# Optimization experiments

Hardware: AMD Instinct MI355X
Metric: run time of the kernel (lower is better)

Reference implementation:

```python
import jax, jax.numpy as jnp
import numpy as np

N, D, S, K = 4096, 256, 32, 4   # nodes, in_dim(=out_dim), subspace_dim, num_heads
ETA = 0.5
LAMBDA_SPARSE = 0.05
EDGE_P = 0.02  # graph density for the random adjacency mask


def setup_inputs() -> dict:
    key = jax.random.key(0)
    k1, k2, k3 = jax.random.split(key, 3)
    H = jax.random.normal(k1, (N, D), dtype=jnp.float32)
    # binary adjacency mask with self-loops, stored as float (matches torch usage)
    mask = (jax.random.uniform(k2, (N, N)) < EDGE_P).astype(jnp.float32)
    adj_mask = jnp.maximum(mask, jnp.eye(N, dtype=jnp.float32))
    # per-head orthonormal subspace bases U[k] = qr(randn(D,S)) -> [K, D, S]
    raw = jax.random.normal(k3, (K, D, S), dtype=jnp.float32)
    U, _ = jnp.linalg.qr(raw)
    log_precision = jnp.zeros((K, S), dtype=jnp.float32)
    threshold = jnp.full((D,), LAMBDA_SPARSE, dtype=jnp.float32)
    return {"H": H, "adj_mask": adj_mask, "U": U,
            "log_precision": log_precision, "threshold": threshold}


def reference(H, adj_mask, U, log_precision, threshold):
    s = U.shape[-1]
    inv_sqrt_s = 1.0 / jnp.sqrt(jnp.asarray(s, dtype=H.dtype))
    neg = (1.0 - adj_mask) * (-1e9)  # [N, N] additive mask

    # scan over heads keeps peak memory at one [N,N] score matrix at a time
    def head_step(agg, xs):
        Uk, lpk = xs                       # [D,S], [S]
        Z = H @ Uk                         # [N,S]  (= Zk^T in the torch code)
        Zs = Z * jnp.exp(lpk)              # precision-scaled
        scores = (Zs @ Z.T) * inv_sqrt_s + neg   # [N,N]
        alpha = jax.nn.softmax(scores, axis=-1)
        agg = agg + (alpha @ Z) @ Uk.T     # [N,D] == (Uk @ (Zk @ alpha^T))^T
        return agg, None

    agg, _ = jax.lax.scan(head_step, jnp.zeros_like(H), (U, log_precision))
    H_half = H + ETA * agg                 # in_dim == out_dim -> no proj

    # soft threshold
    H_out = jnp.sign(H_half) * jax.nn.relu(jnp.abs(H_half) - threshold[None, :])

    # orthogonality loss: sum_k ||Uk^T Uk - I||_F^2 + sum_{k<l} ||Uk^T Ul||_F^2
    C = jnp.einsum('kda,ldb->klab', U, U)  # [K,K,S,S] gram blocks (K,S small)
    Kh = U.shape[0]
    I = jnp.eye(s, dtype=U.dtype)
    diag_blocks = C[jnp.arange(Kh), jnp.arange(Kh)]          # [K,S,S]
    orth_loss = ((diag_blocks - I) ** 2).sum()
    upper = jnp.triu(jnp.ones((Kh, Kh), dtype=U.dtype), 1)[:, :, None, None]
    orth_loss = orth_loss + ((C ** 2) * upper).sum()
    return H_out, orth_loss
```

## Files before the change

### kernel.cpp

```cpp
#include <hip/hip_runtime.h>
#include <math.h>

constexpr int NN = 4096;
constexpr int DD = 256;
constexpr int SS = 32;
constexpr int KK = 4;
constexpr int MAXN = 192;
constexpr int SEGMAX = 96;
constexpr float ETA = 0.5f;

#define MEMFENCE() __asm__ volatile("" ::: "memory")

__global__ __launch_bounds__(256) void prep_kernel(
    const float* __restrict__ H, const float* __restrict__ U,
    const float* __restrict__ lp, float* __restrict__ Z,
    float* __restrict__ elp, float* __restrict__ lossp) {
  __shared__ float Hl[16][DD];
  __shared__ float red[4];
  const int tid = threadIdx.x;

  if (blockIdx.x < 1024) {
    const int k = blockIdx.x & 3;
    const int n0 = (blockIdx.x >> 2) * 16;

    const float4* H4 = (const float4*)(H + (size_t)n0 * DD);
    float4* Hl4 = (float4*)&Hl[0][0];
    for (int i = tid; i < 16 * DD / 4; i += 256) Hl4[i] = H4[i];
    __syncthreads();

    const int s = tid & 31;
    const int n_l = (tid >> 5) & 7;
    const float* Uk = U + (size_t)k * DD * SS;
    float acc0 = 0.f, acc1 = 0.f;
#pragma unroll 4
    for (int dq = 0; dq < DD / 4; dq++) {
      const float4 h0 = Hl4[n_l * (DD / 4) + dq];
      const float4 h1 = Hl4[(n_l + 8) * (DD / 4) + dq];
      const float u0 = Uk[(4 * dq + 0) * SS + s];
      const float u1 = Uk[(4 * dq + 1) * SS + s];
      const float u2 = Uk[(4 * dq + 2) * SS + s];
      const float u3 = Uk[(4 * dq + 3) * SS + s];
      acc0 += h0.x * u0 + h0.y * u1 + h0.z * u2 + h0.w * u3;
      acc1 += h1.x * u0 + h1.y * u1 + h1.z * u2 + h1.w * u3;
    }
    Z[((size_t)k * NN + n0 + n_l) * SS + s] = acc0;
    Z[((size_t)k * NN + n0 + n_l + 8) * SS + s] = acc1;
  } else {
    const int pair = blockIdx.x - 1024;
    if (pair == 0 && tid < KK * SS) elp[tid] = expf(lp[tid]);
    const int pk[10] = {0, 0, 0, 0, 1, 1, 1, 2, 2, 3};
    const int pl[10] = {0, 1, 2, 3, 1, 2, 3, 2, 3, 3};
    const int k = pk[pair], l = pl[pair];
    const int b = tid & 31;
    const int a0 = tid >> 5;
    float acc[4] = {0.f, 0.f, 0.f, 0.f};
    for (int d = 0; d < DD; d++) {
      const float ub = U[((size_t)l * DD + d) * SS + b];
#pragma unroll
      for (int j = 0; j < 4; j++)
        acc[j] += U[((size_t)k * DD + d) * SS + a0 + 8 * j] * ub;
    }
    float tot = 0.f;
#pragma unroll
    for (int j = 0; j < 4; j++) {
      const float cv = acc[j] - ((k == l && (a0 + 8 * j) == b) ? 1.0f : 0.0f);
      tot += cv * cv;
    }
#pragma unroll
    for (int off = 32; off >= 1; off >>= 1) tot += __shfl_xor(tot, off);
    if ((tid & 63) == 0) red[tid >> 6] = tot;
    __syncthreads();
    if (tid == 0) lossp[pair] = red[0] + red[1] + red[2] + red[3];
  }
}

__global__ __launch_bounds__(256) void attn_row(
    const float* __restrict__ mask, const float* __restrict__ Z,
    const float* __restrict__ elp, const float* __restrict__ lossp,
    float* __restrict__ AO, float* __restrict__ loss) {
  const int tid = threadIdx.x;
  const int wv = tid >> 6;
  const int lane = tid & 63;
  const int row = blockIdx.x;

  __shared__ int segn[4][SEGMAX];
  __shared__ int segc[4];
  __shared__ int nbr[MAXN];

  if (blockIdx.x == 0 && tid == 0) {
    float t = 0.f;
#pragma unroll
    for (int i = 0; i < 10; i++) t += lossp[i];
    loss[0] = t;
  }

  const float4* m4 = (const float4*)(mask + (size_t)row * NN);
  const unsigned long long lt = (1ULL << lane) - 1ULL;
  int cnt = 0;
#pragma unroll
  for (int it = 0; it < 4; it++) {
    const int i = wv * 256 + it * 64 + lane;
    const float4 v = m4[i];
    unsigned long long b;
    b = __ballot(v.x > 0.5f);
    if (v.x > 0.5f) { const int p = cnt + (int)__popcll(b & lt); if (p < SEGMAX) segn[wv][p] = 4 * i; }
    cnt += (int)__popcll(b);
    b = __ballot(v.y > 0.5f);
    if (v.y > 0.5f) { const int p = cnt + (int)__popcll(b & lt); if (p < SEGMAX) segn[wv][p] = 4 * i + 1; }
    cnt += (int)__popcll(b);
    b = __ballot(v.z > 0.5f);
    if (v.z > 0.5f) { const int p = cnt + (int)__popcll(b & lt); if (p < SEGMAX) segn[wv][p] = 4 * i + 2; }
    cnt += (int)__popcll(b);
    b = __ballot(v.w > 0.5f);
    if (v.w > 0.5f) { const int p = cnt + (int)__popcll(b & lt); if (p < SEGMAX) segn[wv][p] = 4 * i + 3; }
    cnt += (int)__popcll(b);
  }
  if (lane == 0) segc[wv] = min(cnt, SEGMAX);
  MEMFENCE();
  __syncthreads();

  const int c0 = segc[0], c1 = segc[1], c2 = segc[2], c3 = segc[3];
  const int offs[4] = {0, c0, c0 + c1, c0 + c1 + c2};
  const int c = min(c0 + c1 + c2 + c3, MAXN);
  const int myc = segc[wv];
  const int myoff = offs[wv];
  for (int i = lane; i < myc; i += 64) {
    const int p = myoff + i;
    if (p < MAXN) nbr[p] = segn[wv][i];
  }
  MEMFENCE();
  __syncthreads();

  const int k = wv;
  const int p_sub = lane >> 3;
  const int sq = lane & 7;
  const float inv_sqrt_s = 0.17677669529663687f;

  const float4* Zq4 = (const float4*)(Z + ((size_t)k * NN + row) * SS);
  const float4* E4 = (const float4*)(elp + k * SS);
  float4 q4;
  {
    const float4 a = Zq4[sq], e = E4[sq];
    q4.x = a.x * e.x; q4.y = a.y * e.y; q4.z = a.z * e.z; q4.w = a.w * e.w;
  }

  float m = -3.0e38f, l = 0.f;
  float4 oacc = {0.f, 0.f, 0.f, 0.f};
  const float* Zk = Z + (size_t)k * NN * SS;

  for (int p0 = 0; p0 < c; p0 += 8) {
    const int p = p0 + p_sub;
    const bool act = p < c;
    float4 z4 = {0.f, 0.f, 0.f, 0.f};
    if (act) z4 = ((const float4*)(Zk + (size_t)nbr[p] * SS))[sq];
    float dot = q4.x * z4.x + q4.y * z4.y + q4.z * z4.z + q4.w * z4.w;
    dot += __shfl_xor(dot, 1);
    dot += __shfl_xor(dot, 2);
    dot += __shfl_xor(dot, 4);
    dot *= inv_sqrt_s;
    if (!act) dot = -3.0e38f;
    float cm = dot;
    cm = fmaxf(cm, __shfl_xor(cm, 8));
    cm = fmaxf(cm, __shfl_xor(cm, 16));
    cm = fmaxf(cm, __shfl_xor(cm, 32));
    const float mn = fmaxf(m, cm);
    const float alpha = __expf(m - mn);
    const float w = __expf(dot - mn);
    float ws = w;
    ws += __shfl_xor(ws, 8);
    ws += __shfl_xor(ws, 16);
    ws += __shfl_xor(ws, 32);
    l = l * alpha + ws;
    oacc.x = oacc.x * alpha + w * z4.x;
    oacc.y = oacc.y * alpha + w * z4.y;
    oacc.z = oacc.z * alpha + w * z4.z;
    oacc.w = oacc.w * alpha + w * z4.w;
    m = mn;
  }
#pragma unroll
  for (int off = 8; off <= 32; off <<= 1) {
    oacc.x += __shfl_xor(oacc.x, off);
    oacc.y += __shfl_xor(oacc.y, off);
    oacc.z += __shfl_xor(oacc.z, off);
    oacc.w += __shfl_xor(oacc.w, off);
  }
  const float invl = 1.0f / l;
  if (p_sub == 0) {
    float4 o;
    o.x = oacc.x * invl; o.y = oacc.y * invl; o.z = oacc.z * invl; o.w = oacc.w * invl;
    ((float4*)AO)[(size_t)row * (KK * SS / 4) + k * 8 + sq] = o;
  }
}

__global__ __launch_bounds__(256) void epilogue_kernel(
    const float* __restrict__ H, const float* __restrict__ U,
    const float* __restrict__ thr, const float* __restrict__ AO,
    float* __restrict__ Hout) {
  __shared__ float AOl[4][KK * SS];
  const int tid = threadIdx.x;
  const int r0 = blockIdx.x * 4;

  const float4* AO4 = (const float4*)(AO + (size_t)r0 * KK * SS);
  float4* AOl4 = (float4*)&AOl[0][0];
  if (tid < 128) AOl4[tid] = AO4[tid];
  __syncthreads();

  const int d = tid;
  float acc[4] = {0.f, 0.f, 0.f, 0.f};
  const float4* U4 = (const float4*)U;
#pragma unroll
  for (int k = 0; k < KK; k++) {
    const int ubase = (k * DD + d) * (SS / 4);
#pragma unroll
    for (int sq = 0; sq < SS / 4; sq++) {
      const float4 u = U4[ubase + sq];
#pragma unroll
      for (int r = 0; r < 4; r++) {
        const float4 a = AOl4[r * (KK * SS / 4) + k * (SS / 4) + sq];
        acc[r] += u.x * a.x + u.y * a.y + u.z * a.z + u.w * a.w;
      }
    }
  }
  const float tv = thr[d];
#pragma unroll
  for (int r = 0; r < 4; r++) {
    const float h = H[(size_t)(r0 + r) * DD + d] + ETA * acc[r];
    const float ab = fabsf(h) - tv;
    Hout[(size_t)(r0 + r) * DD + d] = (ab > 0.0f) ? copysignf(ab, h) : 0.0f;
  }
}

extern "C" void kernel_launch(void* const* d_in, const int* in_sizes, int n_in,
                              void* d_out, int out_size, void* d_ws, size_t ws_size,
                              hipStream_t stream) {
  const float* H    = (const float*)d_in[0];
  const float* mask = (const float*)d_in[1];
  const float* U    = (const float*)d_in[2];
  const float* lp   = (const float*)d_in[3];
  const float* thr  = (const float*)d_in[4];

  float* Hout = (float*)d_out;
  float* loss = Hout + (size_t)NN * DD;

  float* Z     = (float*)d_ws;
  float* AO    = Z + (size_t)KK * NN * SS;
  float* elp   = AO + (size_t)NN * KK * SS;
  float* lossp = elp + KK * SS;

  prep_kernel<<<1034, 256, 0, stream>>>(H, U, lp, Z, elp, lossp);
  attn_row<<<NN, 256, 0, stream>>>(mask, Z, elp, lossp, AO, loss);
  epilogue_kernel<<<NN / 4, 256, 0, stream>>>(H, U, thr, AO, Hout);
}
```

Measured before the change: 168.2 us.

## Assign one neighbor per lane and use two-pass softmax with transpose-reduce

Rewrites the per-head attention loop in attn_row. Before, 8 neighbors were processed per iteration with 8 lanes per neighbor, using an online softmax and many shuffles. Now each lane holds whole 32-wide Z rows for up to three neighbors (lane, lane+64, lane+128) in registers. It computes the dots locally, does one wave-wide max and sum, and reduces the 32-element outputs with a recursive-halving shuffle transpose. This removes the serial loop and the per-step shuffle chains. In exchange it raises register pressure (q, zA, zB and o arrays), reloads the third neighbor's row, and loads whole rows per lane, which is uncoalesced.

```diff
diff --git a/kernel.cpp b/kernel.cpp
--- a/kernel.cpp
+++ b/kernel.cpp
@@ -132,64 +132,128 @@
   __syncthreads();
 
   const int k = wv;
-  const int p_sub = lane >> 3;
-  const int sq = lane & 7;
   const float inv_sqrt_s = 0.17677669529663687f;
+  const float* Zk = Z + (size_t)k * NN * SS;
 
   const float4* Zq4 = (const float4*)(Z + ((size_t)k * NN + row) * SS);
   const float4* E4 = (const float4*)(elp + k * SS);
-  float4 q4;
+  float q[SS];
+#pragma unroll
+  for (int u = 0; u < 8; u++) {
+    const float4 a = Zq4[u], e = E4[u];
+    q[4 * u + 0] = a.x * e.x; q[4 * u + 1] = a.y * e.y;
+    q[4 * u + 2] = a.z * e.z; q[4 * u + 3] = a.w * e.w;
+  }
+
+  const int pA = lane, pB = lane + 64;
+  const bool aA = pA < c, aB = pB < c;
+  float zA[SS], zB[SS];
+  if (aA) {
+    const float4* r = (const float4*)(Zk + (size_t)nbr[pA] * SS);
+#pragma unroll
+    for (int u = 0; u < 8; u++) {
+      const float4 v = r[u];
+      zA[4 * u] = v.x; zA[4 * u + 1] = v.y; zA[4 * u + 2] = v.z; zA[4 * u + 3] = v.w;
+    }
+  } else {
+#pragma unroll
+    for (int i = 0; i < SS; i++) zA[i] = 0.f;
+  }
+  if (aB) {
+    const float4* r = (const float4*)(Zk + (size_t)nbr[pB] * SS);
+#pragma unroll
+    for (int u = 0; u < 8; u++) {
+      const float4 v = r[u];
+      zB[4 * u] = v.x; zB[4 * u + 1] = v.y; zB[4 * u + 2] = v.z; zB[4 * u + 3] = v.w;
+    }
+  } else {
+#pragma unroll
+    for (int i = 0; i < SS; i++) zB[i] = 0.f;
+  }
+
+  float sA = -3.0e38f, sB = -3.0e38f, sC = -3.0e38f;
   {
-    const float4 a = Zq4[sq], e = E4[sq];
-    q4.x = a.x * e.x; q4.y = a.y * e.y; q4.z = a.z * e.z; q4.w = a.w * e.w;
-  }
-
-  float m = -3.0e38f, l = 0.f;
-  float4 oacc = {0.f, 0.f, 0.f, 0.f};
-  const float* Zk = Z + (size_t)k * NN * SS;
-
-  for (int p0 = 0; p0 < c; p0 += 8) {
-    const int p = p0 + p_sub;
-    const bool act = p < c;
-    float4 z4 = {0.f, 0.f, 0.f, 0.f};
-    if (act) z4 = ((const float4*)(Zk + (size_t)nbr[p] * SS))[sq];
-    float dot = q4.x * z4.x + q4.y * z4.y + q4.z * z4.z + q4.w * z4.w;
-    dot += __shfl_xor(dot, 1);
-    dot += __shfl_xor(dot, 2);
-    dot += __shfl_xor(dot, 4);
-    dot *= inv_sqrt_s;
-    if (!act) dot = -3.0e38f;
-    float cm = dot;
-    cm = fmaxf(cm, __shfl_xor(cm, 8));
-    cm = fmaxf(cm, __shfl_xor(cm, 16));
-    cm = fmaxf(cm, __shfl_xor(cm, 32));
-    const float mn = fmaxf(m, cm);
-    const float alpha = __expf(m - mn);
-    const float w = __expf(dot - mn);
-    float ws = w;
-    ws += __shfl_xor(ws, 8);
-    ws += __shfl_xor(ws, 16);
-    ws += __shfl_xor(ws, 32);
-    l = l * alpha + ws;
-    oacc.x = oacc.x * alpha + w * z4.x;
-    oacc.y = oacc.y * alpha + w * z4.y;
-    oacc.z = oacc.z * alpha + w * z4.z;
-    oacc.w = oacc.w * alpha + w * z4.w;
-    m = mn;
-  }
-#pragma unroll
-  for (int off = 8; off <= 32; off <<= 1) {
-    oacc.x += __shfl_xor(oacc.x, off);
-    oacc.y += __shfl_xor(oacc.y, off);
-    oacc.z += __shfl_xor(oacc.z, off);
-    oacc.w += __shfl_xor(oacc.w, off);
-  }
-  const float invl = 1.0f / l;
-  if (p_sub == 0) {
-    float4 o;
-    o.x = oacc.x * invl; o.y = oacc.y * invl; o.z = oacc.z * invl; o.w = oacc.w * invl;
-    ((float4*)AO)[(size_t)row * (KK * SS / 4) + k * 8 + sq] = o;
-  }
+    float dA = 0.f, dB = 0.f;
+#pragma unroll
+    for (int i = 0; i < SS; i++) { dA += q[i] * zA[i]; dB += q[i] * zB[i]; }
+    if (aA) sA = dA * inv_sqrt_s;
+    if (aB) sB = dB * inv_sqrt_s;
+  }
+  const bool has3 = (c > 128);
+  if (has3) {
+    const int pC = lane + 128;
+    if (pC < c) {
+      const float4* r = (const float4*)(Zk + (size_t)nbr[pC] * SS);
+      float d = 0.f;
+#pragma unroll
+      for (int u = 0; u < 8; u++) {
+        const float4 v = r[u];
+        d += q[4 * u] * v.x + q[4 * u + 1] * v.y + q[4 * u + 2] * v.z + q[4 * u + 3] * v.w;
+      }
+      sC = d * inv_sqrt_s;
+    }
+  }
+
+  float mx = fmaxf(sA, fmaxf(sB, sC));
+#pragma unroll
+  for (int off = 32; off >= 1; off >>= 1) mx = fmaxf(mx, __shfl_xor(mx, off));
+  const float wA = __expf(sA - mx);
+  const float wB = __expf(sB - mx);
+  const float wC = __expf(sC - mx);
+  float sv = wA + wB + wC;
+#pragma unroll
+  for (int off = 32; off >= 1; off >>= 1) sv += __shfl_xor(sv, off);
+  const float invl = 1.0f / sv;
+
+  float o[SS];
+#pragma unroll
+  for (int i = 0; i < SS; i++) o[i] = wA * zA[i] + wB * zB[i];
+  if (has3) {
+    const int pC = lane + 128;
+    if (pC < c) {
+      const float4* r = (const float4*)(Zk + (size_t)nbr[pC] * SS);
+#pragma unroll
+      for (int u = 0; u < 8; u++) {
+        const float4 v = r[u];
+        o[4 * u] += wC * v.x; o[4 * u + 1] += wC * v.y;
+        o[4 * u + 2] += wC * v.z; o[4 * u + 3] += wC * v.w;
+      }
+    }
+  }
+
+#pragma unroll
+  for (int i = 0; i < 16; i++) {
+    const float snd = (lane & 32) ? o[i] : o[i + 16];
+    const float rcv = __shfl_xor(snd, 32);
+    o[i] = ((lane & 32) ? o[i + 16] : o[i]) + rcv;
+  }
+#pragma unroll
+  for (int i = 0; i < 8; i++) {
+    const float snd = (lane & 16) ? o[i] : o[i + 8];
+    const float rcv = __shfl_xor(snd, 16);
+    o[i] = ((lane & 16) ? o[i + 8] : o[i]) + rcv;
+  }
+#pragma unroll
+  for (int i = 0; i < 4; i++) {
+    const float snd = (lane & 8) ? o[i] : o[i + 4];
+    const float rcv = __shfl_xor(snd, 8);
+    o[i] = ((lane & 8) ? o[i + 4] : o[i]) + rcv;
+  }
+#pragma unroll
+  for (int i = 0; i < 2; i++) {
+    const float snd = (lane & 4) ? o[i] : o[i + 2];
+    const float rcv = __shfl_xor(snd, 4);
+    o[i] = ((lane & 4) ? o[i + 2] : o[i]) + rcv;
+  }
+  {
+    const float snd = (lane & 2) ? o[0] : o[1];
+    const float rcv = __shfl_xor(snd, 2);
+    o[0] = ((lane & 2) ? o[1] : o[0]) + rcv;
+  }
+  const float ofin = o[0] + __shfl_xor(o[0], 1);
+
+  if ((lane & 1) == 0)
+    AO[(size_t)row * (KK * SS) + k * SS + (lane >> 1)] = ofin * invl;
 }
 
 __global__ __launch_bounds__(256) void epilogue_kernel(
```

Result: slower. 183.5 us (+9.1%).

## Replace online softmax with two-pass scores-in-LDS softmax in attention rows

Applied to the files above, without the earlier changes.

The per-neighbor online softmax is replaced by three passes. The first computes scores into shared memory while tracking a max, the second exponentiates and sums from LDS, and the third reloads Z rows to accumulate the weighted sum. The loops are also unrolled to two neighbors per iteration. This removes the serial rescale chain and the per-step cross-lane max and sum shuffles, but reads each neighbor's Z row twice from L2 and uses more LDS.

```diff
diff --git a/kernel.cpp b/kernel.cpp
--- a/kernel.cpp
+++ b/kernel.cpp
@@ -86,6 +86,7 @@
   __shared__ int segn[4][SEGMAX];
   __shared__ int segc[4];
   __shared__ int nbr[MAXN];
+  __shared__ float scw[4][MAXN];
 
   if (blockIdx.x == 0 && tid == 0) {
     float t = 0.f;
@@ -135,59 +136,77 @@
   const int p_sub = lane >> 3;
   const int sq = lane & 7;
   const float inv_sqrt_s = 0.17677669529663687f;
-
-  const float4* Zq4 = (const float4*)(Z + ((size_t)k * NN + row) * SS);
-  const float4* E4 = (const float4*)(elp + k * SS);
+  const float* Zk = Z + (size_t)k * NN * SS;
+
   float4 q4;
   {
-    const float4 a = Zq4[sq], e = E4[sq];
+    const float4 a = ((const float4*)(Z + ((size_t)k * NN + row) * SS))[sq];
+    const float4 e = ((const float4*)(elp + k * SS))[sq];
     q4.x = a.x * e.x; q4.y = a.y * e.y; q4.z = a.z * e.z; q4.w = a.w * e.w;
   }
 
-  float m = -3.0e38f, l = 0.f;
-  float4 oacc = {0.f, 0.f, 0.f, 0.f};
-  const float* Zk = Z + (size_t)k * NN * SS;
-
-  for (int p0 = 0; p0 < c; p0 += 8) {
-    const int p = p0 + p_sub;
-    const bool act = p < c;
-    float4 z4 = {0.f, 0.f, 0.f, 0.f};
-    if (act) z4 = ((const float4*)(Zk + (size_t)nbr[p] * SS))[sq];
-    float dot = q4.x * z4.x + q4.y * z4.y + q4.z * z4.z + q4.w * z4.w;
-    dot += __shfl_xor(dot, 1);
-    dot += __shfl_xor(dot, 2);
-    dot += __shfl_xor(dot, 4);
-    dot *= inv_sqrt_s;
-    if (!act) dot = -3.0e38f;
-    float cm = dot;
-    cm = fmaxf(cm, __shfl_xor(cm, 8));
-    cm = fmaxf(cm, __shfl_xor(cm, 16));
-    cm = fmaxf(cm, __shfl_xor(cm, 32));
-    const float mn = fmaxf(m, cm);
-    const float alpha = __expf(m - mn);
-    const float w = __expf(dot - mn);
-    float ws = w;
-    ws += __shfl_xor(ws, 8);
-    ws += __shfl_xor(ws, 16);
-    ws += __shfl_xor(ws, 32);
-    l = l * alpha + ws;
-    oacc.x = oacc.x * alpha + w * z4.x;
-    oacc.y = oacc.y * alpha + w * z4.y;
-    oacc.z = oacc.z * alpha + w * z4.z;
-    oacc.w = oacc.w * alpha + w * z4.w;
-    m = mn;
+  float lmax = -3.0e38f;
+  for (int p0 = 0; p0 < c; p0 += 16) {
+    const int pa = p0 + p_sub;
+    const int pb = pa + 8;
+    const bool aA = pa < c, aB = pb < c;
+    float4 zA = {0.f, 0.f, 0.f, 0.f}, zB = {0.f, 0.f, 0.f, 0.f};
+    if (aA) zA = ((const float4*)(Zk + (size_t)nbr[pa] * SS))[sq];
+    if (aB) zB = ((const float4*)(Zk + (size_t)nbr[pb] * SS))[sq];
+    float dA = q4.x * zA.x + q4.y * zA.y + q4.z * zA.z + q4.w * zA.w;
+    float dB = q4.x * zB.x + q4.y * zB.y + q4.z * zB.z + q4.w * zB.w;
+    dA += __shfl_xor(dA, 1); dB += __shfl_xor(dB, 1);
+    dA += __shfl_xor(dA, 2); dB += __shfl_xor(dB, 2);
+    dA += __shfl_xor(dA, 4); dB += __shfl_xor(dB, 4);
+    dA = aA ? dA * inv_sqrt_s : -3.0e38f;
+    dB = aB ? dB * inv_sqrt_s : -3.0e38f;
+    if (sq == 0 && aA) scw[wv][pa] = dA;
+    if (sq == 0 && aB) scw[wv][pb] = dB;
+    lmax = fmaxf(lmax, fmaxf(dA, dB));
+  }
+  MEMFENCE();
+#pragma unroll
+  for (int off = 32; off >= 1; off >>= 1) lmax = fmaxf(lmax, __shfl_xor(lmax, off));
+
+  float wsum = 0.f;
+#pragma unroll
+  for (int t = 0; t < 3; t++) {
+    const int p = lane + t * 64;
+    if (p < c) {
+      const float w = __expf(scw[wv][p] - lmax);
+      scw[wv][p] = w;
+      wsum += w;
+    }
+  }
+  MEMFENCE();
+#pragma unroll
+  for (int off = 32; off >= 1; off >>= 1) wsum += __shfl_xor(wsum, off);
+  const float invl = 1.0f / wsum;
+
+  float4 o4 = {0.f, 0.f, 0.f, 0.f};
+  for (int p0 = 0; p0 < c; p0 += 16) {
+    const int pa = p0 + p_sub;
+    const int pb = pa + 8;
+    const bool aA = pa < c, aB = pb < c;
+    float wA = 0.f, wB = 0.f;
+    float4 zA = {0.f, 0.f, 0.f, 0.f}, zB = {0.f, 0.f, 0.f, 0.f};
+    if (aA) { wA = scw[wv][pa]; zA = ((const float4*)(Zk + (size_t)nbr[pa] * SS))[sq]; }
+    if (aB) { wB = scw[wv][pb]; zB = ((const float4*)(Zk + (size_t)nbr[pb] * SS))[sq]; }
+    o4.x += wA * zA.x + wB * zB.x;
+    o4.y += wA * zA.y + wB * zB.y;
+    o4.z += wA * zA.z + wB * zB.z;
+    o4.w += wA * zA.w + wB * zB.w;
   }
 #pragma unroll
   for (int off = 8; off <= 32; off <<= 1) {
-    oacc.x += __shfl_xor(oacc.x, off);
-    oacc.y += __shfl_xor(oacc.y, off);
-    oacc.z += __shfl_xor(oacc.z, off);
-    oacc.w += __shfl_xor(oacc.w, off);
-  }
-  const float invl = 1.0f / l;
+    o4.x += __shfl_xor(o4.x, off);
+    o4.y += __shfl_xor(o4.y, off);
+    o4.z += __shfl_xor(o4.z, off);
+    o4.w += __shfl_xor(o4.w, off);
+  }
   if (p_sub == 0) {
     float4 o;
-    o.x = oacc.x * invl; o.y = oacc.y * invl; o.z = oacc.z * invl; o.w = oacc.w * invl;
+    o.x = o4.x * invl; o.y = o4.y * invl; o.z = o4.z * invl; o.w = o4.w * invl;
     ((float4*)AO)[(size_t)row * (KK * SS / 4) + k * 8 + sq] = o;
   }
 }
```

Result: faster. 164.4 us (-2.3%).
